# Kernel tuning notes

Hardware: AMD Instinct MI355X
Metric: run time of the kernel (lower is better)

The kernel has to match this reference:

```python
import jax, jax.numpy as jnp
import numpy as np

B, L, D = 32, 128, 512

def setup_inputs() -> dict:
    key = jax.random.key(0)
    ks = jax.random.split(key, 10)
    s = 1.0 / np.sqrt(D)
    return {
        "current_sotw": jax.random.normal(ks[0], (B, L, D), jnp.float32),
        "new_obs": jax.random.normal(ks[1], (B, L, D), jnp.float32),
        "Wq": jax.random.uniform(ks[2], (D, D), jnp.float32, -s, s),   # linear_query weight
        "bq": jax.random.uniform(ks[3], (D,), jnp.float32, -s, s),     # linear_query bias
        "Wc": jax.random.uniform(ks[4], (D, D), jnp.float32, -s, s),   # linear_context (no bias)
        "v": jax.random.uniform(ks[5], (D,), jnp.float32, -s, s),      # v projection to scalar score
        "Wout": jax.random.uniform(ks[6], (2 * D, D), jnp.float32, -s, s),  # linear_out weight
        "bout": jax.random.uniform(ks[7], (D,), jnp.float32, -s, s),        # linear_out bias (mlp type)
        "mix": jax.random.uniform(ks[8], (1,), jnp.float32),           # mixing_proportion ~ U[0,1)
    }

def _global_attn_mlp(source, memory, Wq, bq, Wc, v, Wout, bout):
    # OpenNMT GlobalAttention, attn_type='mlp', attn_func='softmax'
    wq = jnp.einsum('btd,de->bte', source, Wq) + bq          # [B,T,D]
    uh = jnp.einsum('bsd,de->bse', memory, Wc)               # [B,S,D]
    # scores: v . tanh(wq + uh) over broadcast [B,T,S,D]
    scores = jnp.einsum('btsd,d->bts', jnp.tanh(wq[:, :, None, :] + uh[:, None, :, :]), v)
    align = jax.nn.softmax(scores, axis=-1)                  # [B,T,S]
    c = jnp.einsum('bts,bsd->btd', align, memory)            # context [B,T,D]
    attn_h = jnp.einsum('btd,de->bte', jnp.concatenate([c, source], axis=-1), Wout) + bout
    return attn_h  # [B,T,D] (the torch code transposes to [T,B,D] then back)

def reference(current_sotw, new_obs, Wq, bq, Wc, v, Wout, bout, mix):
    a1 = _global_attn_mlp(new_obs, current_sotw, Wq, bq, Wc, v, Wout, bout)
    a2 = _global_attn_mlp(current_sotw, new_obs, Wq, bq, Wc, v, Wout, bout)
    m = mix[0]
    return (1.0 - m) * a1 + m * a2
```

## Files before the change

### kernel.cpp

```cpp
#include <hip/hip_runtime.h>

#define DD 512
#define SS 128
#define TT 16
#define SCH 16
#define C2F 2.8853900817779268f
#define L2EF 1.4426950408889634f

typedef __bf16 bf16x8 __attribute__((ext_vector_type(8)));
typedef float f32x4 __attribute__((ext_vector_type(4)));
typedef unsigned int uint32x4 __attribute__((ext_vector_type(4)));

__device__ __forceinline__ unsigned short f2bf(float f) {
    unsigned int u = __builtin_bit_cast(unsigned int, f);
    u += 0x7fffu + ((u >> 16) & 1u);
    return (unsigned short)(u >> 16);
}
__device__ __forceinline__ float bflo(unsigned int u) { return __builtin_bit_cast(float, u << 16); }
__device__ __forceinline__ float bfhi(unsigned int u) { return __builtin_bit_cast(float, u & 0xffff0000u); }

__global__ __launch_bounds__(256)
void f32_to_bf16_k(const float* __restrict__ in, unsigned short* __restrict__ out, int n8)
{
    int i = blockIdx.x * 256 + threadIdx.x;
    if (i < n8) {
        const float4 a = ((const float4*)in)[2 * i];
        const float4 b = ((const float4*)in)[2 * i + 1];
        uint32x4 o;
        o[0] = (unsigned)f2bf(a.x) | ((unsigned)f2bf(a.y) << 16);
        o[1] = (unsigned)f2bf(a.z) | ((unsigned)f2bf(a.w) << 16);
        o[2] = (unsigned)f2bf(b.x) | ((unsigned)f2bf(b.y) << 16);
        o[3] = (unsigned)f2bf(b.z) | ((unsigned)f2bf(b.w) << 16);
        ((uint32x4*)out)[i] = o;
    }
}

__global__ __launch_bounds__(256)
void transpose_bf16(const float* __restrict__ in, unsigned short* __restrict__ out, int R, int C)
{
    __shared__ float t[64][65];
    const int r0 = blockIdx.y * 64, c0 = blockIdx.x * 64;
    const int tid = threadIdx.x;
    const int lc = tid & 63, lr = tid >> 6;
    #pragma unroll
    for (int i = 0; i < 16; ++i) {
        int r = lr + i * 4;
        t[r][lc] = in[(size_t)(r0 + r) * C + c0 + lc];
    }
    __syncthreads();
    #pragma unroll
    for (int i = 0; i < 16; ++i) {
        int rr = lr + i * 4;
        out[(size_t)(c0 + rr) * R + r0 + lc] = f2bf(t[lc][rr]);
    }
}

template<int K, bool OUT_BF16, bool SCALE>
__global__ __launch_bounds__(256)
void gemm_mfma(const unsigned short* __restrict__ A, const unsigned short* __restrict__ Bt,
               const float* __restrict__ bias, void* __restrict__ Cout, int N)
{
    constexpr int BM = 128, BN = 64, BK = 64, LDA = BK + 8;
    __shared__ __align__(16) unsigned short As[BM][LDA];
    __shared__ __align__(16) unsigned short Bs[BN][LDA];

    const int tid = threadIdx.x;
    const int m0 = blockIdx.y * BM, n0 = blockIdx.x * BN;
    const int lane = tid & 63, wid = tid >> 6;
    const int wr = wid >> 1, wc = wid & 1;
    const int lr = lane & 15, kb = lane >> 4;

    f32x4 acc[4][2] = {};
    uint32x4 ra[4], rb[2];

    auto LOADK = [&](int k0) {
        #pragma unroll
        for (int j = 0; j < 4; ++j) {
            int id = tid + 256 * j; int r = id >> 3, s = id & 7;
            ra[j] = *(const uint32x4*)&A[(size_t)(m0 + r) * K + k0 + s * 8];
        }
        #pragma unroll
        for (int j = 0; j < 2; ++j) {
            int id = tid + 256 * j; int r = id >> 3, s = id & 7;
            rb[j] = *(const uint32x4*)&Bt[(size_t)(n0 + r) * K + k0 + s * 8];
        }
    };

    LOADK(0);
    #pragma unroll 1
    for (int step = 0; step < K / BK; ++step) {
        __syncthreads();
        #pragma unroll
        for (int j = 0; j < 4; ++j) {
            int id = tid + 256 * j; int r = id >> 3, s = id & 7;
            *(uint32x4*)&As[r][s * 8] = ra[j];
        }
        #pragma unroll
        for (int j = 0; j < 2; ++j) {
            int id = tid + 256 * j; int r = id >> 3, s = id & 7;
            *(uint32x4*)&Bs[r][s * 8] = rb[j];
        }
        __syncthreads();
        if (step + 1 < K / BK) LOADK((step + 1) * BK);
        #pragma unroll
        for (int kk = 0; kk < BK; kk += 32) {
            bf16x8 b0 = __builtin_bit_cast(bf16x8, *(const uint32x4*)&Bs[wc * 32 + lr][kk + kb * 8]);
            bf16x8 b1 = __builtin_bit_cast(bf16x8, *(const uint32x4*)&Bs[wc * 32 + 16 + lr][kk + kb * 8]);
            #pragma unroll
            for (int mf = 0; mf < 4; ++mf) {
                bf16x8 a0 = __builtin_bit_cast(bf16x8, *(const uint32x4*)&As[wr * 64 + mf * 16 + lr][kk + kb * 8]);
                acc[mf][0] = __builtin_amdgcn_mfma_f32_16x16x32_bf16(a0, b0, acc[mf][0], 0, 0, 0);
                acc[mf][1] = __builtin_amdgcn_mfma_f32_16x16x32_bf16(a0, b1, acc[mf][1], 0, 0, 0);
            }
        }
    }

    #pragma unroll
    for (int nf = 0; nf < 2; ++nf) {
        const int col = n0 + wc * 32 + nf * 16 + lr;
        const float bv = bias ? bias[col] : 0.0f;
        #pragma unroll
        for (int mf = 0; mf < 4; ++mf) {
            const int row = m0 + wr * 64 + mf * 16 + kb * 4;
            #pragma unroll
            for (int r = 0; r < 4; ++r) {
                float valf = acc[mf][nf][r] + bv;
                if (SCALE) valf *= C2F;
                if (OUT_BF16) ((unsigned short*)Cout)[(size_t)(row + r) * N + col] = f2bf(valf);
                else          ((float*)Cout)[(size_t)(row + r) * N + col] = valf;
            }
        }
    }
}

__global__ __launch_bounds__(512, 6)
void attn_fused(const unsigned short* __restrict__ wq,
                const unsigned short* __restrict__ uh,
                const float* __restrict__ v,
                const float* __restrict__ mem,
                unsigned short* __restrict__ c_out)
{
    __shared__ __align__(16) unsigned short s_wq[TT][DD + 8];
    __shared__ __align__(16) unsigned short s_uh[SCH][DD + 8];
    __shared__ float s_v2[DD];
    __shared__ float s_sc[TT * SS];

    const int b = blockIdx.y;
    const int t0 = blockIdx.x * TT;
    const int tid = threadIdx.x;

    {
        const uint32x4* wp = (const uint32x4*)(wq + ((size_t)b * SS + t0) * DD);
        for (int i = tid; i < TT * 64; i += 512) {
            int row = i >> 6, c8 = i & 63;
            *(uint32x4*)&s_wq[row][c8 * 8] = wp[row * 64 + c8];
        }
        for (int i = tid; i < DD; i += 512) s_v2[i] = v[i] * 2.0f;
    }

    const int t  = (tid >> 1) & 15;
    const int sr = (tid >> 5) & 15;
    const int hh = tid & 1;

    for (int sc0 = 0; sc0 < SS; sc0 += SCH) {
        __syncthreads();
        const uint32x4* up = (const uint32x4*)(uh + ((size_t)b * SS + sc0) * DD);
        for (int i = tid; i < SCH * 64; i += 512) {
            int row = i >> 6, c8 = i & 63;
            *(uint32x4*)&s_uh[row][c8 * 8] = up[row * 64 + c8];
        }
        __syncthreads();

        const unsigned int* wrow = (const unsigned int*)&s_wq[t][hh * 256];
        const unsigned int* urow = (const unsigned int*)&s_uh[sr][hh * 256];
        const float* v2 = &s_v2[hh * 256];

        float a0 = 0.f, a1 = 0.f, a2 = 0.f, a3 = 0.f;
        #pragma unroll 2
        for (int j = 0; j < 128; j += 4) {
            uint32x4 w4 = *(const uint32x4*)&wrow[j];
            uint32x4 u4 = *(const uint32x4*)&urow[j];
            const float4 vA = *(const float4*)&v2[2 * j];
            const float4 vB = *(const float4*)&v2[2 * j + 4];
            float x, e;
            x = fmaf(C2F, bflo(u4[0]), bflo(w4[0])); e = __builtin_amdgcn_exp2f(x);
            a0 = fmaf(vA.x, __builtin_amdgcn_rcpf(e + 1.f), a0);
            x = fmaf(C2F, bfhi(u4[0]), bfhi(w4[0])); e = __builtin_amdgcn_exp2f(x);
            a1 = fmaf(vA.y, __builtin_amdgcn_rcpf(e + 1.f), a1);
            x = fmaf(C2F, bflo(u4[1]), bflo(w4[1])); e = __builtin_amdgcn_exp2f(x);
            a2 = fmaf(vA.z, __builtin_amdgcn_rcpf(e + 1.f), a2);
            x = fmaf(C2F, bfhi(u4[1]), bfhi(w4[1])); e = __builtin_amdgcn_exp2f(x);
            a3 = fmaf(vA.w, __builtin_amdgcn_rcpf(e + 1.f), a3);
            x = fmaf(C2F, bflo(u4[2]), bflo(w4[2])); e = __builtin_amdgcn_exp2f(x);
            a0 = fmaf(vB.x, __builtin_amdgcn_rcpf(e + 1.f), a0);
            x = fmaf(C2F, bfhi(u4[2]), bfhi(w4[2])); e = __builtin_amdgcn_exp2f(x);
            a1 = fmaf(vB.y, __builtin_amdgcn_rcpf(e + 1.f), a1);
            x = fmaf(C2F, bflo(u4[3]), bflo(w4[3])); e = __builtin_amdgcn_exp2f(x);
            a2 = fmaf(vB.z, __builtin_amdgcn_rcpf(e + 1.f), a2);
            x = fmaf(C2F, bfhi(u4[3]), bfhi(w4[3])); e = __builtin_amdgcn_exp2f(x);
            a3 = fmaf(vB.w, __builtin_amdgcn_rcpf(e + 1.f), a3);
        }
        float partial = (a0 + a1) + (a2 + a3);
        partial += __shfl_xor(partial, 1);
        if (hh == 0) s_sc[t * SS + sc0 + sr] = -partial;
    }
    __syncthreads();

    {
        const int tr  = tid >> 5;
        const int l32 = tid & 31;
        float x0 = s_sc[tr * SS + l32];
        float x1 = s_sc[tr * SS + l32 + 32];
        float x2 = s_sc[tr * SS + l32 + 64];
        float x3 = s_sc[tr * SS + l32 + 96];
        float mx = fmaxf(fmaxf(x0, x1), fmaxf(x2, x3));
        #pragma unroll
        for (int off = 16; off > 0; off >>= 1) mx = fmaxf(mx, __shfl_xor(mx, off));
        const float e0 = __builtin_amdgcn_exp2f((x0 - mx) * L2EF);
        const float e1 = __builtin_amdgcn_exp2f((x1 - mx) * L2EF);
        const float e2 = __builtin_amdgcn_exp2f((x2 - mx) * L2EF);
        const float e3 = __builtin_amdgcn_exp2f((x3 - mx) * L2EF);
        float sum = (e0 + e1) + (e2 + e3);
        #pragma unroll
        for (int off = 16; off > 0; off >>= 1) sum += __shfl_xor(sum, off);
        const float rs = __builtin_amdgcn_rcpf(sum);
        __syncthreads();
        s_sc[tr * SS + l32]      = e0 * rs;
        s_sc[tr * SS + l32 + 32] = e1 * rs;
        s_sc[tr * SS + l32 + 64] = e2 * rs;
        s_sc[tr * SS + l32 + 96] = e3 * rs;
    }
    __syncthreads();

    {
        const int w    = tid >> 6;
        const int lane = tid & 63;
        const int tg   = w >> 1;
        const int hf   = w & 1;
        const int d    = hf * 256 + lane * 4;
        const float* mb = mem + (size_t)b * SS * DD;

        float4 ac0 = {0,0,0,0}, ac1 = {0,0,0,0}, ac2 = {0,0,0,0}, ac3 = {0,0,0,0};
        for (int s = 0; s < SS; ++s) {
            const float4 mv = *(const float4*)&mb[(size_t)s * DD + d];
            const float e0 = s_sc[(tg * 4 + 0) * SS + s];
            const float e1 = s_sc[(tg * 4 + 1) * SS + s];
            const float e2 = s_sc[(tg * 4 + 2) * SS + s];
            const float e3 = s_sc[(tg * 4 + 3) * SS + s];
            ac0.x = fmaf(e0, mv.x, ac0.x); ac0.y = fmaf(e0, mv.y, ac0.y);
            ac0.z = fmaf(e0, mv.z, ac0.z); ac0.w = fmaf(e0, mv.w, ac0.w);
            ac1.x = fmaf(e1, mv.x, ac1.x); ac1.y = fmaf(e1, mv.y, ac1.y);
            ac1.z = fmaf(e1, mv.z, ac1.z); ac1.w = fmaf(e1, mv.w, ac1.w);
            ac2.x = fmaf(e2, mv.x, ac2.x); ac2.y = fmaf(e2, mv.y, ac2.y);
            ac2.z = fmaf(e2, mv.z, ac2.z); ac2.w = fmaf(e2, mv.w, ac2.w);
            ac3.x = fmaf(e3, mv.x, ac3.x); ac3.y = fmaf(e3, mv.y, ac3.y);
            ac3.z = fmaf(e3, mv.z, ac3.z); ac3.w = fmaf(e3, mv.w, ac3.w);
        }
        unsigned short* cp = c_out + ((size_t)b * SS + t0 + tg * 4) * DD + d;
        uint2 st;
        st.x = (unsigned)f2bf(ac0.x) | ((unsigned)f2bf(ac0.y) << 16);
        st.y = (unsigned)f2bf(ac0.z) | ((unsigned)f2bf(ac0.w) << 16);
        *(uint2*)&cp[0 * DD] = st;
        st.x = (unsigned)f2bf(ac1.x) | ((unsigned)f2bf(ac1.y) << 16);
        st.y = (unsigned)f2bf(ac1.z) | ((unsigned)f2bf(ac1.w) << 16);
        *(uint2*)&cp[1 * DD] = st;
        st.x = (unsigned)f2bf(ac2.x) | ((unsigned)f2bf(ac2.y) << 16);
        st.y = (unsigned)f2bf(ac2.z) | ((unsigned)f2bf(ac2.w) << 16);
        *(uint2*)&cp[2 * DD] = st;
        st.x = (unsigned)f2bf(ac3.x) | ((unsigned)f2bf(ac3.y) << 16);
        st.y = (unsigned)f2bf(ac3.z) | ((unsigned)f2bf(ac3.w) << 16);
        *(uint2*)&cp[3 * DD] = st;
    }
}

__global__ __launch_bounds__(256)
void mix_cat(const unsigned short* __restrict__ c1, const unsigned short* __restrict__ c2,
             const float* __restrict__ s1, const float* __restrict__ s2,
             const float* __restrict__ mix, unsigned short* __restrict__ Acat, int M)
{
    const float m = mix[0], om = 1.0f - m;
    const int idx = blockIdx.x * 256 + threadIdx.x;
    const int row = idx >> 7;
    const int col = (idx & 127) * 4;
    if (row >= M) return;
    const size_t p = (size_t)row * 512 + col;
    const uint2 c1v = *(const uint2*)&c1[p];
    const uint2 c2v = *(const uint2*)&c2[p];
    const float4 s1v = *(const float4*)&s1[p];
    const float4 s2v = *(const float4*)&s2[p];
    uint2 o;
    float x0 = om * bflo(c1v.x) + m * bflo(c2v.x);
    float x1 = om * bfhi(c1v.x) + m * bfhi(c2v.x);
    float x2 = om * bflo(c1v.y) + m * bflo(c2v.y);
    float x3 = om * bfhi(c1v.y) + m * bfhi(c2v.y);
    o.x = (unsigned)f2bf(x0) | ((unsigned)f2bf(x1) << 16);
    o.y = (unsigned)f2bf(x2) | ((unsigned)f2bf(x3) << 16);
    *(uint2*)&Acat[(size_t)row * 1024 + col] = o;
    x0 = om * s1v.x + m * s2v.x;
    x1 = om * s1v.y + m * s2v.y;
    x2 = om * s1v.z + m * s2v.z;
    x3 = om * s1v.w + m * s2v.w;
    o.x = (unsigned)f2bf(x0) | ((unsigned)f2bf(x1) << 16);
    o.y = (unsigned)f2bf(x2) | ((unsigned)f2bf(x3) << 16);
    *(uint2*)&Acat[(size_t)row * 1024 + 512 + col] = o;
}

extern "C" void kernel_launch(void* const* d_in, const int* in_sizes, int n_in,
                              void* d_out, int out_size, void* d_ws, size_t ws_size,
                              hipStream_t stream) {
    const float* cs   = (const float*)d_in[0];
    const float* no   = (const float*)d_in[1];
    const float* Wq   = (const float*)d_in[2];
    const float* bq   = (const float*)d_in[3];
    const float* Wc   = (const float*)d_in[4];
    const float* v    = (const float*)d_in[5];
    const float* Wout = (const float*)d_in[6];
    const float* bout = (const float*)d_in[7];
    const float* mix  = (const float*)d_in[8];
    float* out = (float*)d_out;

    const int B = 32, L = 128, M = B * L;
    typedef unsigned short us;
    char* ws = (char*)d_ws;
    us* cs_bf  = (us*)(ws);
    us* no_bf  = (us*)(ws + (4u << 20));
    us* Wqt    = (us*)(ws + (8u << 20));
    us* Wct    = (us*)(ws + (8u << 20) + (512u << 10));
    us* Woutt  = (us*)(ws + (9u << 20));
    us* wq_bf  = (us*)(ws + (10u << 20));
    us* uh_bf  = (us*)(ws + (14u << 20));
    us* c1_bf  = (us*)(ws + (18u << 20));
    us* c2_bf  = (us*)(ws + (22u << 20));
    us* Acat   = (us*)(ws + (10u << 20));

    const dim3 b256(256);
    const int n8 = M * DD / 8;

    f32_to_bf16_k<<<dim3(n8 / 256), b256, 0, stream>>>(cs, cs_bf, n8);
    f32_to_bf16_k<<<dim3(n8 / 256), b256, 0, stream>>>(no, no_bf, n8);
    transpose_bf16<<<dim3(8, 8),  b256, 0, stream>>>(Wq,   Wqt,   512, 512);
    transpose_bf16<<<dim3(8, 8),  b256, 0, stream>>>(Wc,   Wct,   512, 512);
    transpose_bf16<<<dim3(8, 16), b256, 0, stream>>>(Wout, Woutt, 1024, 512);

    const dim3 gg(DD / 64, M / 128);
    const dim3 ga(L / TT, B);

    gemm_mfma<512, true, true ><<<gg, b256, 0, stream>>>(no_bf, Wqt, bq,      (void*)wq_bf, DD);
    gemm_mfma<512, true, false><<<gg, b256, 0, stream>>>(cs_bf, Wct, nullptr, (void*)uh_bf, DD);
    attn_fused<<<ga, dim3(512), 0, stream>>>(wq_bf, uh_bf, v, cs, c1_bf);

    gemm_mfma<512, true, true ><<<gg, b256, 0, stream>>>(cs_bf, Wqt, bq,      (void*)wq_bf, DD);
    gemm_mfma<512, true, false><<<gg, b256, 0, stream>>>(no_bf, Wct, nullptr, (void*)uh_bf, DD);
    attn_fused<<<ga, dim3(512), 0, stream>>>(wq_bf, uh_bf, v, no, c2_bf);

    mix_cat<<<dim3(M * 128 / 256), b256, 0, stream>>>(c1_bf, c2_bf, no, cs, mix, Acat, M);
    gemm_mfma<1024, false, false><<<gg, b256, 0, stream>>>(Acat, Woutt, bout, (void*)out, DD);
}
```

Baseline: 317.6 us.

## Fuse projection GEMMs, retile attention, fold mix into final GEMM loader

The Wq and Wc projections now share one concatenated weight, so each input needs a single N=1024 GEMM that writes both wq and uh. The attention kernel drops from 16 to 4 query rows per block for more blocks, uses a permuted shared-memory layout with 8-way lane splits and shuffle reductions, and reads memory rows as bf16 staged through shared memory instead of fp32 from global. The mix_cat kernel is removed and its blend is folded into the A-tile loader of the final GEMM, saving one launch and the Acat round trip. The trade-offs are that attention now recomputes score-tile loads across four times as many blocks, and the context reduction uses bf16 memory values.

```diff
diff --git a/kernel.cpp b/kernel.cpp
--- a/kernel.cpp
+++ b/kernel.cpp
@@ -2,8 +2,9 @@
 
 #define DD 512
 #define SS 128
-#define TT 16
-#define SCH 16
+#define TT4 4
+#define SCH16 16
+#define RW 520
 #define C2F 2.8853900817779268f
 #define L2EF 1.4426950408889634f
 
@@ -55,60 +56,54 @@
     }
 }
 
-template<int K, bool OUT_BF16, bool SCALE>
 __global__ __launch_bounds__(256)
-void gemm_mfma(const unsigned short* __restrict__ A, const unsigned short* __restrict__ Bt,
-               const float* __restrict__ bias, void* __restrict__ Cout, int N)
+void gemm_proj(const unsigned short* __restrict__ A,
+               const unsigned short* __restrict__ Bt,
+               const float* __restrict__ bq,
+               unsigned short* __restrict__ outW,
+               unsigned short* __restrict__ outU)
 {
-    constexpr int BM = 128, BN = 64, BK = 64, LDA = BK + 8;
-    __shared__ __align__(16) unsigned short As[BM][LDA];
-    __shared__ __align__(16) unsigned short Bs[BN][LDA];
+    constexpr int K = 512, LDA = 72;
+    __shared__ __align__(16) unsigned short As[64][LDA];
+    __shared__ __align__(16) unsigned short Bs[64][LDA];
 
     const int tid = threadIdx.x;
-    const int m0 = blockIdx.y * BM, n0 = blockIdx.x * BN;
+    const int n0 = blockIdx.x * 64, m0 = blockIdx.y * 64;
     const int lane = tid & 63, wid = tid >> 6;
     const int wr = wid >> 1, wc = wid & 1;
     const int lr = lane & 15, kb = lane >> 4;
 
-    f32x4 acc[4][2] = {};
-    uint32x4 ra[4], rb[2];
+    f32x4 acc[2][2] = {};
+    uint32x4 ra[2], rb[2];
 
     auto LOADK = [&](int k0) {
         #pragma unroll
-        for (int j = 0; j < 4; ++j) {
+        for (int j = 0; j < 2; ++j) {
             int id = tid + 256 * j; int r = id >> 3, s = id & 7;
             ra[j] = *(const uint32x4*)&A[(size_t)(m0 + r) * K + k0 + s * 8];
-        }
+            rb[j] = *(const uint32x4*)&Bt[(size_t)(n0 + r) * K + k0 + s * 8];
+        }
+    };
+
+    LOADK(0);
+    #pragma unroll 1
+    for (int step = 0; step < K / 64; ++step) {
+        __syncthreads();
         #pragma unroll
         for (int j = 0; j < 2; ++j) {
             int id = tid + 256 * j; int r = id >> 3, s = id & 7;
-            rb[j] = *(const uint32x4*)&Bt[(size_t)(n0 + r) * K + k0 + s * 8];
-        }
-    };
-
-    LOADK(0);
-    #pragma unroll 1
-    for (int step = 0; step < K / BK; ++step) {
-        __syncthreads();
-        #pragma unroll
-        for (int j = 0; j < 4; ++j) {
-            int id = tid + 256 * j; int r = id >> 3, s = id & 7;
             *(uint32x4*)&As[r][s * 8] = ra[j];
-        }
-        #pragma unroll
-        for (int j = 0; j < 2; ++j) {
-            int id = tid + 256 * j; int r = id >> 3, s = id & 7;
             *(uint32x4*)&Bs[r][s * 8] = rb[j];
         }
         __syncthreads();
-        if (step + 1 < K / BK) LOADK((step + 1) * BK);
-        #pragma unroll
-        for (int kk = 0; kk < BK; kk += 32) {
+        if (step + 1 < K / 64) LOADK((step + 1) * 64);
+        #pragma unroll
+        for (int kk = 0; kk < 64; kk += 32) {
             bf16x8 b0 = __builtin_bit_cast(bf16x8, *(const uint32x4*)&Bs[wc * 32 + lr][kk + kb * 8]);
             bf16x8 b1 = __builtin_bit_cast(bf16x8, *(const uint32x4*)&Bs[wc * 32 + 16 + lr][kk + kb * 8]);
             #pragma unroll
-            for (int mf = 0; mf < 4; ++mf) {
-                bf16x8 a0 = __builtin_bit_cast(bf16x8, *(const uint32x4*)&As[wr * 64 + mf * 16 + lr][kk + kb * 8]);
+            for (int mf = 0; mf < 2; ++mf) {
+                bf16x8 a0 = __builtin_bit_cast(bf16x8, *(const uint32x4*)&As[wr * 32 + mf * 16 + lr][kk + kb * 8]);
                 acc[mf][0] = __builtin_amdgcn_mfma_f32_16x16x32_bf16(a0, b0, acc[mf][0], 0, 0, 0);
                 acc[mf][1] = __builtin_amdgcn_mfma_f32_16x16x32_bf16(a0, b1, acc[mf][1], 0, 0, 0);
             }
@@ -118,70 +113,166 @@
     #pragma unroll
     for (int nf = 0; nf < 2; ++nf) {
         const int col = n0 + wc * 32 + nf * 16 + lr;
-        const float bv = bias ? bias[col] : 0.0f;
-        #pragma unroll
-        for (int mf = 0; mf < 4; ++mf) {
-            const int row = m0 + wr * 64 + mf * 16 + kb * 4;
+        #pragma unroll
+        for (int mf = 0; mf < 2; ++mf) {
+            const int row = m0 + wr * 32 + mf * 16 + kb * 4;
             #pragma unroll
             for (int r = 0; r < 4; ++r) {
-                float valf = acc[mf][nf][r] + bv;
-                if (SCALE) valf *= C2F;
-                if (OUT_BF16) ((unsigned short*)Cout)[(size_t)(row + r) * N + col] = f2bf(valf);
-                else          ((float*)Cout)[(size_t)(row + r) * N + col] = valf;
-            }
-        }
-    }
-}
-
-__global__ __launch_bounds__(512, 6)
+                const float valf = acc[mf][nf][r];
+                if (col < 512) outW[(size_t)(row + r) * 512 + col] = f2bf((valf + bq[col]) * C2F);
+                else           outU[(size_t)(row + r) * 512 + (col - 512)] = f2bf(valf);
+            }
+        }
+    }
+}
+
+__global__ __launch_bounds__(256)
+void gemm_final(const unsigned short* __restrict__ c1, const unsigned short* __restrict__ c2,
+                const float* __restrict__ no, const float* __restrict__ cs,
+                const float* __restrict__ mix,
+                const unsigned short* __restrict__ Bt,
+                const float* __restrict__ bout, float* __restrict__ out)
+{
+    constexpr int K = 1024, LDA = 72;
+    __shared__ __align__(16) unsigned short As[64][LDA];
+    __shared__ __align__(16) unsigned short Bs[64][LDA];
+
+    const int tid = threadIdx.x;
+    const int n0 = blockIdx.x * 64, m0 = blockIdx.y * 64;
+    const int lane = tid & 63, wid = tid >> 6;
+    const int wr = wid >> 1, wc = wid & 1;
+    const int lr = lane & 15, kb = lane >> 4;
+    const float mxv = mix[0], omv = 1.0f - mxv;
+
+    f32x4 acc[2][2] = {};
+    uint32x4 ra[2], rb[2];
+
+    auto LOADK = [&](int k0) {
+        #pragma unroll
+        for (int j = 0; j < 2; ++j) {
+            int id = tid + 256 * j; int r = id >> 3, s = id & 7;
+            const size_t row = m0 + r;
+            const int k = k0 + s * 8;
+            uint32x4 o;
+            if (k < 512) {
+                const uint32x4 x1 = *(const uint32x4*)&c1[row * 512 + k];
+                const uint32x4 x2 = *(const uint32x4*)&c2[row * 512 + k];
+                #pragma unroll
+                for (int q = 0; q < 4; ++q) {
+                    float lo = omv * bflo(x1[q]) + mxv * bflo(x2[q]);
+                    float hi = omv * bfhi(x1[q]) + mxv * bfhi(x2[q]);
+                    o[q] = (unsigned)f2bf(lo) | ((unsigned)f2bf(hi) << 16);
+                }
+            } else {
+                const float* n1 = &no[row * 512 + k - 512];
+                const float* s1 = &cs[row * 512 + k - 512];
+                const float4 a1 = *(const float4*)n1, a2 = *(const float4*)(n1 + 4);
+                const float4 b1 = *(const float4*)s1, b2 = *(const float4*)(s1 + 4);
+                o[0] = (unsigned)f2bf(omv * a1.x + mxv * b1.x) | ((unsigned)f2bf(omv * a1.y + mxv * b1.y) << 16);
+                o[1] = (unsigned)f2bf(omv * a1.z + mxv * b1.z) | ((unsigned)f2bf(omv * a1.w + mxv * b1.w) << 16);
+                o[2] = (unsigned)f2bf(omv * a2.x + mxv * b2.x) | ((unsigned)f2bf(omv * a2.y + mxv * b2.y) << 16);
+                o[3] = (unsigned)f2bf(omv * a2.z + mxv * b2.z) | ((unsigned)f2bf(omv * a2.w + mxv * b2.w) << 16);
+            }
+            ra[j] = o;
+            rb[j] = *(const uint32x4*)&Bt[(size_t)(n0 + r) * K + k0 + s * 8];
+        }
+    };
+
+    LOADK(0);
+    #pragma unroll 1
+    for (int step = 0; step < K / 64; ++step) {
+        __syncthreads();
+        #pragma unroll
+        for (int j = 0; j < 2; ++j) {
+            int id = tid + 256 * j; int r = id >> 3, s = id & 7;
+            *(uint32x4*)&As[r][s * 8] = ra[j];
+            *(uint32x4*)&Bs[r][s * 8] = rb[j];
+        }
+        __syncthreads();
+        if (step + 1 < K / 64) LOADK((step + 1) * 64);
+        #pragma unroll
+        for (int kk = 0; kk < 64; kk += 32) {
+            bf16x8 b0 = __builtin_bit_cast(bf16x8, *(const uint32x4*)&Bs[wc * 32 + lr][kk + kb * 8]);
+            bf16x8 b1 = __builtin_bit_cast(bf16x8, *(const uint32x4*)&Bs[wc * 32 + 16 + lr][kk + kb * 8]);
+            #pragma unroll
+            for (int mf = 0; mf < 2; ++mf) {
+                bf16x8 a0 = __builtin_bit_cast(bf16x8, *(const uint32x4*)&As[wr * 32 + mf * 16 + lr][kk + kb * 8]);
+                acc[mf][0] = __builtin_amdgcn_mfma_f32_16x16x32_bf16(a0, b0, acc[mf][0], 0, 0, 0);
+                acc[mf][1] = __builtin_amdgcn_mfma_f32_16x16x32_bf16(a0, b1, acc[mf][1], 0, 0, 0);
+            }
+        }
+    }
+
+    #pragma unroll
+    for (int nf = 0; nf < 2; ++nf) {
+        const int col = n0 + wc * 32 + nf * 16 + lr;
+        const float bv = bout[col];
+        #pragma unroll
+        for (int mf = 0; mf < 2; ++mf) {
+            const int row = m0 + wr * 32 + mf * 16 + kb * 4;
+            #pragma unroll
+            for (int r = 0; r < 4; ++r)
+                out[(size_t)(row + r) * 512 + col] = acc[mf][nf][r] + bv;
+        }
+    }
+}
+
+__global__ __launch_bounds__(512, 8)
 void attn_fused(const unsigned short* __restrict__ wq,
                 const unsigned short* __restrict__ uh,
                 const float* __restrict__ v,
-                const float* __restrict__ mem,
+                const unsigned short* __restrict__ mem,
                 unsigned short* __restrict__ c_out)
 {
-    __shared__ __align__(16) unsigned short s_wq[TT][DD + 8];
-    __shared__ __align__(16) unsigned short s_uh[SCH][DD + 8];
-    __shared__ float s_v2[DD];
-    __shared__ float s_sc[TT * SS];
-
-    const int b = blockIdx.y;
-    const int t0 = blockIdx.x * TT;
+    __shared__ __align__(16) unsigned short s_wq[TT4 * RW];
+    __shared__ __align__(16) unsigned short s_uh[SCH16 * RW];
+    __shared__ __align__(16) float s_v2[DD];
+    __shared__ float s_sc[TT4 * SS];
+
+    const int b = blockIdx.y, t0 = blockIdx.x * TT4;
     const int tid = threadIdx.x;
 
-    {
-        const uint32x4* wp = (const uint32x4*)(wq + ((size_t)b * SS + t0) * DD);
-        for (int i = tid; i < TT * 64; i += 512) {
-            int row = i >> 6, c8 = i & 63;
-            *(uint32x4*)&s_wq[row][c8 * 8] = wp[row * 64 + c8];
-        }
-        for (int i = tid; i < DD; i += 512) s_v2[i] = v[i] * 2.0f;
-    }
-
-    const int t  = (tid >> 1) & 15;
-    const int sr = (tid >> 5) & 15;
-    const int hh = tid & 1;
-
-    for (int sc0 = 0; sc0 < SS; sc0 += SCH) {
-        __syncthreads();
-        const uint32x4* up = (const uint32x4*)(uh + ((size_t)b * SS + sc0) * DD);
-        for (int i = tid; i < SCH * 64; i += 512) {
-            int row = i >> 6, c8 = i & 63;
-            *(uint32x4*)&s_uh[row][c8 * 8] = up[row * 64 + c8];
-        }
-        __syncthreads();
-
-        const unsigned int* wrow = (const unsigned int*)&s_wq[t][hh * 256];
-        const unsigned int* urow = (const unsigned int*)&s_uh[sr][hh * 256];
-        const float* v2 = &s_v2[hh * 256];
+    if (tid < 256) {
+        const int row = tid >> 6, G = tid & 63;
+        const int P = ((G & 7) << 3) | (G >> 3);
+        *(uint32x4*)&s_wq[row * RW + P * 8] =
+            *(const uint32x4*)&wq[((size_t)b * SS + t0 + row) * DD + G * 8];
+    } else if (tid < 384) {
+        const int H = tid - 256;
+        const int P = ((H & 15) << 3) | (H >> 4);
+        float4 val = *(const float4*)&v[H * 4];
+        val.x *= 2.f; val.y *= 2.f; val.z *= 2.f; val.w *= 2.f;
+        *(float4*)&s_v2[P * 4] = val;
+    }
+
+    const int oct = tid & 7;
+    const int sr  = (tid >> 3) & 15;
+    const int t   = tid >> 7;
+
+    for (int sc0 = 0; sc0 < SS; sc0 += SCH16) {
+        __syncthreads();
+        {
+            int i = tid;
+            #pragma unroll
+            for (int rep = 0; rep < 2; ++rep, i += 512) {
+                const int row = i >> 6, G = i & 63;
+                const int P = ((G & 7) << 3) | (G >> 3);
+                *(uint32x4*)&s_uh[row * RW + P * 8] =
+                    *(const uint32x4*)&uh[((size_t)b * SS + sc0 + row) * DD + G * 8];
+            }
+        }
+        __syncthreads();
+
+        const unsigned short* wrow = &s_wq[t * RW];
+        const unsigned short* urow = &s_uh[sr * RW];
 
         float a0 = 0.f, a1 = 0.f, a2 = 0.f, a3 = 0.f;
-        #pragma unroll 2
-        for (int j = 0; j < 128; j += 4) {
-            uint32x4 w4 = *(const uint32x4*)&wrow[j];
-            uint32x4 u4 = *(const uint32x4*)&urow[j];
-            const float4 vA = *(const float4*)&v2[2 * j];
-            const float4 vB = *(const float4*)&v2[2 * j + 4];
+        #pragma unroll 4
+        for (int j = 0; j < 8; ++j) {
+            const uint32x4 w4 = *(const uint32x4*)&wrow[(8 * j + oct) * 8];
+            const uint32x4 u4 = *(const uint32x4*)&urow[(8 * j + oct) * 8];
+            const float4 vA = *(const float4*)&s_v2[(16 * j + oct) * 4];
+            const float4 vB = *(const float4*)&s_v2[(16 * j + 8 + oct) * 4];
             float x, e;
             x = fmaf(C2F, bflo(u4[0]), bflo(w4[0])); e = __builtin_amdgcn_exp2f(x);
             a0 = fmaf(vA.x, __builtin_amdgcn_rcpf(e + 1.f), a0);
@@ -200,15 +291,16 @@
             x = fmaf(C2F, bfhi(u4[3]), bfhi(w4[3])); e = __builtin_amdgcn_exp2f(x);
             a3 = fmaf(vB.w, __builtin_amdgcn_rcpf(e + 1.f), a3);
         }
-        float partial = (a0 + a1) + (a2 + a3);
-        partial += __shfl_xor(partial, 1);
-        if (hh == 0) s_sc[t * SS + sc0 + sr] = -partial;
+        float p = (a0 + a1) + (a2 + a3);
+        p += __shfl_xor(p, 1);
+        p += __shfl_xor(p, 2);
+        p += __shfl_xor(p, 4);
+        if (oct == 0) s_sc[t * SS + sc0 + sr] = -p;
     }
     __syncthreads();
 
-    {
-        const int tr  = tid >> 5;
-        const int l32 = tid & 31;
+    if (tid < 128) {
+        const int tr = tid >> 5, l32 = tid & 31;
         float x0 = s_sc[tr * SS + l32];
         float x1 = s_sc[tr * SS + l32 + 32];
         float x2 = s_sc[tr * SS + l32 + 64];
@@ -224,85 +316,43 @@
         #pragma unroll
         for (int off = 16; off > 0; off >>= 1) sum += __shfl_xor(sum, off);
         const float rs = __builtin_amdgcn_rcpf(sum);
-        __syncthreads();
         s_sc[tr * SS + l32]      = e0 * rs;
         s_sc[tr * SS + l32 + 32] = e1 * rs;
         s_sc[tr * SS + l32 + 64] = e2 * rs;
         s_sc[tr * SS + l32 + 96] = e3 * rs;
     }
-    __syncthreads();
-
-    {
-        const int w    = tid >> 6;
-        const int lane = tid & 63;
-        const int tg   = w >> 1;
-        const int hf   = w & 1;
-        const int d    = hf * 256 + lane * 4;
-        const float* mb = mem + (size_t)b * SS * DD;
-
-        float4 ac0 = {0,0,0,0}, ac1 = {0,0,0,0}, ac2 = {0,0,0,0}, ac3 = {0,0,0,0};
-        for (int s = 0; s < SS; ++s) {
-            const float4 mv = *(const float4*)&mb[(size_t)s * DD + d];
-            const float e0 = s_sc[(tg * 4 + 0) * SS + s];
-            const float e1 = s_sc[(tg * 4 + 1) * SS + s];
-            const float e2 = s_sc[(tg * 4 + 2) * SS + s];
-            const float e3 = s_sc[(tg * 4 + 3) * SS + s];
-            ac0.x = fmaf(e0, mv.x, ac0.x); ac0.y = fmaf(e0, mv.y, ac0.y);
-            ac0.z = fmaf(e0, mv.z, ac0.z); ac0.w = fmaf(e0, mv.w, ac0.w);
-            ac1.x = fmaf(e1, mv.x, ac1.x); ac1.y = fmaf(e1, mv.y, ac1.y);
-            ac1.z = fmaf(e1, mv.z, ac1.z); ac1.w = fmaf(e1, mv.w, ac1.w);
-            ac2.x = fmaf(e2, mv.x, ac2.x); ac2.y = fmaf(e2, mv.y, ac2.y);
-            ac2.z = fmaf(e2, mv.z, ac2.z); ac2.w = fmaf(e2, mv.w, ac2.w);
-            ac3.x = fmaf(e3, mv.x, ac3.x); ac3.y = fmaf(e3, mv.y, ac3.y);
-            ac3.z = fmaf(e3, mv.z, ac3.z); ac3.w = fmaf(e3, mv.w, ac3.w);
-        }
-        unsigned short* cp = c_out + ((size_t)b * SS + t0 + tg * 4) * DD + d;
-        uint2 st;
-        st.x = (unsigned)f2bf(ac0.x) | ((unsigned)f2bf(ac0.y) << 16);
-        st.y = (unsigned)f2bf(ac0.z) | ((unsigned)f2bf(ac0.w) << 16);
-        *(uint2*)&cp[0 * DD] = st;
-        st.x = (unsigned)f2bf(ac1.x) | ((unsigned)f2bf(ac1.y) << 16);
-        st.y = (unsigned)f2bf(ac1.z) | ((unsigned)f2bf(ac1.w) << 16);
-        *(uint2*)&cp[1 * DD] = st;
-        st.x = (unsigned)f2bf(ac2.x) | ((unsigned)f2bf(ac2.y) << 16);
-        st.y = (unsigned)f2bf(ac2.z) | ((unsigned)f2bf(ac2.w) << 16);
-        *(uint2*)&cp[2 * DD] = st;
-        st.x = (unsigned)f2bf(ac3.x) | ((unsigned)f2bf(ac3.y) << 16);
-        st.y = (unsigned)f2bf(ac3.z) | ((unsigned)f2bf(ac3.w) << 16);
-        *(uint2*)&cp[3 * DD] = st;
-    }
-}
-
-__global__ __launch_bounds__(256)
-void mix_cat(const unsigned short* __restrict__ c1, const unsigned short* __restrict__ c2,
-             const float* __restrict__ s1, const float* __restrict__ s2,
-             const float* __restrict__ mix, unsigned short* __restrict__ Acat, int M)
-{
-    const float m = mix[0], om = 1.0f - m;
-    const int idx = blockIdx.x * 256 + threadIdx.x;
-    const int row = idx >> 7;
-    const int col = (idx & 127) * 4;
-    if (row >= M) return;
-    const size_t p = (size_t)row * 512 + col;
-    const uint2 c1v = *(const uint2*)&c1[p];
-    const uint2 c2v = *(const uint2*)&c2[p];
-    const float4 s1v = *(const float4*)&s1[p];
-    const float4 s2v = *(const float4*)&s2[p];
-    uint2 o;
-    float x0 = om * bflo(c1v.x) + m * bflo(c2v.x);
-    float x1 = om * bfhi(c1v.x) + m * bfhi(c2v.x);
-    float x2 = om * bflo(c1v.y) + m * bflo(c2v.y);
-    float x3 = om * bfhi(c1v.y) + m * bfhi(c2v.y);
-    o.x = (unsigned)f2bf(x0) | ((unsigned)f2bf(x1) << 16);
-    o.y = (unsigned)f2bf(x2) | ((unsigned)f2bf(x3) << 16);
-    *(uint2*)&Acat[(size_t)row * 1024 + col] = o;
-    x0 = om * s1v.x + m * s2v.x;
-    x1 = om * s1v.y + m * s2v.y;
-    x2 = om * s1v.z + m * s2v.z;
-    x3 = om * s1v.w + m * s2v.w;
-    o.x = (unsigned)f2bf(x0) | ((unsigned)f2bf(x1) << 16);
-    o.y = (unsigned)f2bf(x2) | ((unsigned)f2bf(x3) << 16);
-    *(uint2*)&Acat[(size_t)row * 1024 + 512 + col] = o;
+
+    const int w = tid >> 6, lane = tid & 63;
+    const int tb = w & 3, half = w >> 2;
+    const int d = half * 256 + lane * 4;
+    f32x4 ac = {0.f, 0.f, 0.f, 0.f};
+
+    for (int sc0 = 0; sc0 < SS; sc0 += SCH16) {
+        __syncthreads();
+        {
+            int i = tid;
+            #pragma unroll
+            for (int rep = 0; rep < 2; ++rep, i += 512) {
+                const int row = i >> 6, G = i & 63;
+                *(uint32x4*)&s_uh[row * RW + G * 8] =
+                    *(const uint32x4*)&mem[((size_t)b * SS + sc0 + row) * DD + G * 8];
+            }
+        }
+        __syncthreads();
+        #pragma unroll
+        for (int srow = 0; srow < SCH16; ++srow) {
+            const float e = s_sc[tb * SS + sc0 + srow];
+            const uint2 mv = *(const uint2*)&s_uh[srow * RW + d];
+            ac[0] = fmaf(e, bflo(mv.x), ac[0]);
+            ac[1] = fmaf(e, bfhi(mv.x), ac[1]);
+            ac[2] = fmaf(e, bflo(mv.y), ac[2]);
+            ac[3] = fmaf(e, bfhi(mv.y), ac[3]);
+        }
+    }
+    uint2 st;
+    st.x = (unsigned)f2bf(ac[0]) | ((unsigned)f2bf(ac[1]) << 16);
+    st.y = (unsigned)f2bf(ac[2]) | ((unsigned)f2bf(ac[3]) << 16);
+    *(uint2*)&c_out[((size_t)b * SS + t0 + tb) * DD + d] = st;
 }
 
 extern "C" void kernel_launch(void* const* d_in, const int* in_sizes, int n_in,
@@ -319,40 +369,33 @@
     const float* mix  = (const float*)d_in[8];
     float* out = (float*)d_out;
 
-    const int B = 32, L = 128, M = B * L;
     typedef unsigned short us;
     char* ws = (char*)d_ws;
-    us* cs_bf  = (us*)(ws);
-    us* no_bf  = (us*)(ws + (4u << 20));
-    us* Wqt    = (us*)(ws + (8u << 20));
-    us* Wct    = (us*)(ws + (8u << 20) + (512u << 10));
-    us* Woutt  = (us*)(ws + (9u << 20));
-    us* wq_bf  = (us*)(ws + (10u << 20));
-    us* uh_bf  = (us*)(ws + (14u << 20));
-    us* c1_bf  = (us*)(ws + (18u << 20));
-    us* c2_bf  = (us*)(ws + (22u << 20));
-    us* Acat   = (us*)(ws + (10u << 20));
+    us* cs_bf = (us*)(ws);
+    us* no_bf = (us*)(ws + (4u  << 20));
+    us* Wqct  = (us*)(ws + (8u  << 20));
+    us* Woutt = (us*)(ws + (9u  << 20));
+    us* wq1   = (us*)(ws + (10u << 20));
+    us* uh2   = (us*)(ws + (14u << 20));
+    us* wq2   = (us*)(ws + (18u << 20));
+    us* uh1   = (us*)(ws + (22u << 20));
+    us* c1    = (us*)(ws + (26u << 20));
+    us* c2    = (us*)(ws + (10u << 20));
 
     const dim3 b256(256);
-    const int n8 = M * DD / 8;
+    const int n8 = 4096 * DD / 8;
 
     f32_to_bf16_k<<<dim3(n8 / 256), b256, 0, stream>>>(cs, cs_bf, n8);
     f32_to_bf16_k<<<dim3(n8 / 256), b256, 0, stream>>>(no, no_bf, n8);
-    transpose_bf16<<<dim3(8, 8),  b256, 0, stream>>>(Wq,   Wqt,   512, 512);
-    transpose_bf16<<<dim3(8, 8),  b256, 0, stream>>>(Wc,   Wct,   512, 512);
+    transpose_bf16<<<dim3(8, 8),  b256, 0, stream>>>(Wq, Wqct, 512, 512);
+    transpose_bf16<<<dim3(8, 8),  b256, 0, stream>>>(Wc, Wqct + 512 * 512, 512, 512);
     transpose_bf16<<<dim3(8, 16), b256, 0, stream>>>(Wout, Woutt, 1024, 512);
 
-    const dim3 gg(DD / 64, M / 128);
-    const dim3 ga(L / TT, B);
-
-    gemm_mfma<512, true, true ><<<gg, b256, 0, stream>>>(no_bf, Wqt, bq,      (void*)wq_bf, DD);
-    gemm_mfma<512, true, false><<<gg, b256, 0, stream>>>(cs_bf, Wct, nullptr, (void*)uh_bf, DD);
-    attn_fused<<<ga, dim3(512), 0, stream>>>(wq_bf, uh_bf, v, cs, c1_bf);
-
-    gemm_mfma<512, true, true ><<<gg, b256, 0, stream>>>(cs_bf, Wqt, bq,      (void*)wq_bf, DD);
-    gemm_mfma<512, true, false><<<gg, b256, 0, stream>>>(no_bf, Wct, nullptr, (void*)uh_bf, DD);
-    attn_fused<<<ga, dim3(512), 0, stream>>>(wq_bf, uh_bf, v, no, c2_bf);
-
-    mix_cat<<<dim3(M * 128 / 256), b256, 0, stream>>>(c1_bf, c2_bf, no, cs, mix, Acat, M);
-    gemm_mfma<1024, false, false><<<gg, b256, 0, stream>>>(Acat, Woutt, bout, (void*)out, DD);
-}
+    gemm_proj<<<dim3(16, 64), b256, 0, stream>>>(no_bf, Wqct, bq, wq1, uh2);
+    gemm_proj<<<dim3(16, 64), b256, 0, stream>>>(cs_bf, Wqct, bq, wq2, uh1);
+
+    attn_fused<<<dim3(32, 32), dim3(512), 0, stream>>>(wq1, uh1, v, cs_bf, c1);
+    attn_fused<<<dim3(32, 32), dim3(512), 0, stream>>>(wq2, uh2, v, no_bf, c2);
+
+    gemm_final<<<dim3(8, 64), b256, 0, stream>>>(c1, c2, no, cs, mix, Woutt, bout, out);
+}
```

Result: slower. 333.5 us (+5.0%).
